# Kernel tuning notes

Hardware: AMD Instinct MI355X
Metric: run time of the kernel (lower is better)

Reference implementation:

```python
import jax, jax.numpy as jnp
import numpy as np

TEMPERATURE = 1.0
EPS = 1e-8
B, D, N, K = 2048, 32, 8192, 30


def setup_inputs() -> dict:
    key = jax.random.key(0)
    k1, k2, k3 = jax.random.split(key, 3)
    z_current = jax.random.normal(k1, (B, D), dtype=jnp.float32)
    pre_knn_indices = jax.random.randint(k2, (N, K), 0, N, dtype=jnp.int64 if jax.config.jax_enable_x64 else jnp.int32)
    sample_indices = jax.random.randint(k3, (B,), 0, N, dtype=jnp.int64 if jax.config.jax_enable_x64 else jnp.int32)
    return {"z_current": z_current, "pre_knn_indices": pre_knn_indices, "sample_indices": sample_indices}


def reference(z_current, pre_knn_indices, sample_indices):
    b = z_current.shape[0]
    eye = jnp.eye(b, dtype=bool)
    # pairwise Euclidean distance via gram trick: (B,B), avoids (B,B,D) intermediate
    sq = jnp.sum(z_current * z_current, axis=-1)
    d2 = jnp.maximum(sq[:, None] + sq[None, :] - 2.0 * (z_current @ z_current.T), 0.0)
    d2_safe = jnp.where(eye, 1.0, d2)  # avoid sqrt(0) on diagonal (masked below anyway)
    dist = jnp.sqrt(d2_safe)
    sim = jnp.where(eye, -jnp.inf, -dist / TEMPERATURE)
    soft_neighbors = jax.nn.softmax(sim, axis=1)  # (B,B)
    # neighbor mask: j is kept iff global id of j is in pre-kNN set of i, and j != i
    knn = pre_knn_indices[sample_indices]  # (B,K) global ids of i's pre-neighbors
    in_set = (knn[:, :, None] == sample_indices[None, None, :]).any(axis=1)  # (B,B)
    mask = in_set & ~eye
    s = jnp.sum(soft_neighbors * mask, axis=1)  # (B,)
    valid = mask.any(axis=1)
    count = valid.sum()
    loss_i = -jnp.log(s + EPS)
    total = jnp.sum(jnp.where(valid, loss_i, 0.0))
    return jnp.where(count > 0, total / count, jnp.float32(0.0))
```

## Files before the change

kernel.cpp:

```cpp
#include <hip/hip_runtime.h>
#include <math.h>

#define Bsz 2048
#define Ddim 32
#define Nsz 8192
#define Kk 30
#define TPB 256
#define ROWS 4
#define JSL 2
#define JTILE (Bsz / JSL)
#define JCH (JTILE / TPB)
#define NBLK ((Bsz / ROWS) * JSL)
#define NW (Nsz / 32)

__global__ __launch_bounds__(TPB, 2) void softnp_main(
    const float* __restrict__ z,
    const int*   __restrict__ pre_knn,
    const int*   __restrict__ samp,
    float*       __restrict__ wsden,
    float*       __restrict__ wsnum)
{
    __shared__ unsigned bits4[NW][ROWS];
    __shared__ int      sampsh[JTILE];
    __shared__ float    zish[ROWS * Ddim];
    __shared__ int      rowsi[ROWS];
    __shared__ float    rden[4][ROWS], rnum[4][ROWS];

    const int t  = threadIdx.x;
    const int rg = blockIdx.x >> 1;
    const int sl = blockIdx.x & 1;
    const int i0 = rg * ROWS;
    const int jb = sl * JTILE;

    #pragma unroll
    for (int c = 0; c < (NW * ROWS) / TPB; ++c)
        ((unsigned*)bits4)[t + c * TPB] = 0u;
    #pragma unroll
    for (int c = 0; c < JCH; ++c)
        sampsh[t + c * TPB] = samp[jb + t + c * TPB];
    if (t < ROWS * Ddim) zish[t] = z[(size_t)i0 * Ddim + t];
    if (t < ROWS) rowsi[t] = samp[i0 + t];
    __syncthreads();

    if (t < ROWS * 32) {
        const int r = t >> 5, k = t & 31;
        if (k < Kk) {
            const int id = pre_knn[(size_t)rowsi[r] * Kk + k];
            atomicOr(&bits4[id >> 5][r], 1u << (id & 31));
        }
    }

    float4 zi[ROWS][Ddim / 4];
    const float4* z4 = (const float4*)zish;
    #pragma unroll
    for (int r = 0; r < ROWS; ++r)
        #pragma unroll
        for (int d = 0; d < Ddim / 4; ++d)
            zi[r][d] = z4[r * (Ddim / 4) + d];

    float si2[ROWS];
    #pragma unroll
    for (int r = 0; r < ROWS; ++r) {
        float s = 0.f;
        #pragma unroll
        for (int d = 0; d < Ddim / 4; ++d)
            s += zi[r][d].x * zi[r][d].x + zi[r][d].y * zi[r][d].y
               + zi[r][d].z * zi[r][d].z + zi[r][d].w * zi[r][d].w;
        si2[r] = s;
    }
    __syncthreads();

    float den[ROWS] = {0.f, 0.f, 0.f, 0.f};
    float num[ROWS] = {0.f, 0.f, 0.f, 0.f};

    const float4* zg = (const float4*)z;
    int j = jb + t;
    float4 cur[8];
    #pragma unroll
    for (int d = 0; d < 8; ++d) cur[d] = zg[(size_t)j * 8 + d];

    #pragma unroll
    for (int c = 0; c < JCH; ++c) {
        float4 nxt[8];
        if (c + 1 < JCH) {
            #pragma unroll
            for (int d = 0; d < 8; ++d) nxt[d] = zg[(size_t)(j + TPB) * 8 + d];
        }

        float dot[ROWS] = {0.f, 0.f, 0.f, 0.f};
        float sj2 = 0.f;
        #pragma unroll
        for (int d = 0; d < 8; ++d) {
            const float4 v = cur[d];
            sj2 += v.x * v.x + v.y * v.y + v.z * v.z + v.w * v.w;
            #pragma unroll
            for (int r = 0; r < ROWS; ++r)
                dot[r] += zi[r][d].x * v.x + zi[r][d].y * v.y
                        + zi[r][d].z * v.z + zi[r][d].w * v.w;
        }

        const int   sj = sampsh[t + c * TPB];
        const uint4 bw = ((const uint4*)bits4)[sj >> 5];
        const unsigned bsel[4] = {bw.x, bw.y, bw.z, bw.w};
        #pragma unroll
        for (int r = 0; r < ROWS; ++r) {
            const float d2 = fmaxf(si2[r] + sj2 - 2.f * dot[r], 0.f);
            const bool diag = (j == i0 + r);
            const float e = diag ? 0.f : __expf(-sqrtf(d2));
            den[r] += e;
            if (!diag && ((bsel[r] >> (sj & 31)) & 1u)) num[r] += e;
        }

        if (c + 1 < JCH) {
            #pragma unroll
            for (int d = 0; d < 8; ++d) cur[d] = nxt[d];
        }
        j += TPB;
    }

    const int lane = t & 63, wv = t >> 6;
    #pragma unroll
    for (int r = 0; r < ROWS; ++r) {
        #pragma unroll
        for (int off = 32; off > 0; off >>= 1) {
            den[r] += __shfl_xor(den[r], off, 64);
            num[r] += __shfl_xor(num[r], off, 64);
        }
    }
    if (lane == 0) {
        #pragma unroll
        for (int r = 0; r < ROWS; ++r) { rden[wv][r] = den[r]; rnum[wv][r] = num[r]; }
    }
    __syncthreads();

    if (t < ROWS) {
        float D = 0.f, Nm = 0.f;
        #pragma unroll
        for (int w = 0; w < 4; ++w) { D += rden[w][t]; Nm += rnum[w][t]; }
        wsden[sl * Bsz + i0 + t] = D;
        wsnum[sl * Bsz + i0 + t] = Nm;
    }
}

__global__ __launch_bounds__(TPB) void softnp_final(
    const float* __restrict__ wsden,
    const float* __restrict__ wsnum,
    float*       __restrict__ out)
{
    __shared__ float rl[4], rc[4];
    const int t = threadIdx.x;
    float loss = 0.f, vcnt = 0.f;
    #pragma unroll
    for (int c = 0; c < Bsz / TPB; ++c) {
        const int r = t + c * TPB;
        const float D  = wsden[r] + wsden[Bsz + r];
        const float Nm = wsnum[r] + wsnum[Bsz + r];
        if (Nm > 0.f) {
            loss -= __logf(Nm / D + 1e-8f);
            vcnt += 1.f;
        }
    }
    #pragma unroll
    for (int off = 32; off > 0; off >>= 1) {
        loss += __shfl_xor(loss, off, 64);
        vcnt += __shfl_xor(vcnt, off, 64);
    }
    const int lane = t & 63, wv = t >> 6;
    if (lane == 0) { rl[wv] = loss; rc[wv] = vcnt; }
    __syncthreads();
    if (t == 0) {
        const float L = rl[0] + rl[1] + rl[2] + rl[3];
        const float C = rc[0] + rc[1] + rc[2] + rc[3];
        out[0] = (C > 0.f) ? L / C : 0.f;
    }
}

extern "C" void kernel_launch(void* const* d_in, const int* in_sizes, int n_in,
                              void* d_out, int out_size, void* d_ws, size_t ws_size,
                              hipStream_t stream)
{
    const float* z       = (const float*)d_in[0];
    const int*   pre_knn = (const int*)d_in[1];
    const int*   samp    = (const int*)d_in[2];
    float*       out     = (float*)d_out;
    float*       wsden   = (float*)d_ws;
    float*       wsnum   = wsden + JSL * Bsz;

    softnp_main<<<dim3(NBLK), dim3(TPB), 0, stream>>>(z, pre_knn, samp, wsden, wsnum);
    softnp_final<<<dim3(1), dim3(TPB), 0, stream>>>(wsden, wsnum, out);
}
```

Baseline: 85.55 us.

## Drop column split; compute per-row loss in main kernel, prefetch sample ids

Removes the two-way column split so each block covers all 2048 columns for its 4 rows. That halves the grid to 512 blocks and drops the redundant per-block bitmask build and z-row loads. The log-loss and valid count are now computed per row inside the main kernel and reduced per block, so the final kernel only sums 512 partials. Sample ids are prefetched from global memory into registers alongside z instead of being staged in shared memory. The trade-off is fewer blocks, which may underfill the 256 CUs on MI355X at 2 blocks per CU and lengthens each block's serial loop.

```diff
diff --git a/kernel.cpp b/kernel.cpp
--- a/kernel.cpp
+++ b/kernel.cpp
@@ -7,37 +7,28 @@
 #define Kk 30
 #define TPB 256
 #define ROWS 4
-#define JSL 2
-#define JTILE (Bsz / JSL)
-#define JCH (JTILE / TPB)
-#define NBLK ((Bsz / ROWS) * JSL)
+#define JCH (Bsz / TPB)
+#define NBLK (Bsz / ROWS)
 #define NW (Nsz / 32)
 
 __global__ __launch_bounds__(TPB, 2) void softnp_main(
     const float* __restrict__ z,
     const int*   __restrict__ pre_knn,
     const int*   __restrict__ samp,
-    float*       __restrict__ wsden,
-    float*       __restrict__ wsnum)
+    float*       __restrict__ wsloss,
+    float*       __restrict__ wscnt)
 {
     __shared__ unsigned bits4[NW][ROWS];
-    __shared__ int      sampsh[JTILE];
     __shared__ float    zish[ROWS * Ddim];
     __shared__ int      rowsi[ROWS];
     __shared__ float    rden[4][ROWS], rnum[4][ROWS];
 
     const int t  = threadIdx.x;
-    const int rg = blockIdx.x >> 1;
-    const int sl = blockIdx.x & 1;
-    const int i0 = rg * ROWS;
-    const int jb = sl * JTILE;
+    const int i0 = blockIdx.x * ROWS;
 
     #pragma unroll
     for (int c = 0; c < (NW * ROWS) / TPB; ++c)
         ((unsigned*)bits4)[t + c * TPB] = 0u;
-    #pragma unroll
-    for (int c = 0; c < JCH; ++c)
-        sampsh[t + c * TPB] = samp[jb + t + c * TPB];
     if (t < ROWS * Ddim) zish[t] = z[(size_t)i0 * Ddim + t];
     if (t < ROWS) rowsi[t] = samp[i0 + t];
     __syncthreads();
@@ -51,12 +42,12 @@
     }
 
     float4 zi[ROWS][Ddim / 4];
-    const float4* z4 = (const float4*)zish;
+    const float4* z4s = (const float4*)zish;
     #pragma unroll
     for (int r = 0; r < ROWS; ++r)
         #pragma unroll
         for (int d = 0; d < Ddim / 4; ++d)
-            zi[r][d] = z4[r * (Ddim / 4) + d];
+            zi[r][d] = z4s[r * (Ddim / 4) + d];
 
     float si2[ROWS];
     #pragma unroll
@@ -74,17 +65,20 @@
     float num[ROWS] = {0.f, 0.f, 0.f, 0.f};
 
     const float4* zg = (const float4*)z;
-    int j = jb + t;
+    int j = t;
     float4 cur[8];
     #pragma unroll
     for (int d = 0; d < 8; ++d) cur[d] = zg[(size_t)j * 8 + d];
+    int scur = samp[j];
 
     #pragma unroll
     for (int c = 0; c < JCH; ++c) {
         float4 nxt[8];
+        int snxt = 0;
         if (c + 1 < JCH) {
             #pragma unroll
             for (int d = 0; d < 8; ++d) nxt[d] = zg[(size_t)(j + TPB) * 8 + d];
+            snxt = samp[j + TPB];
         }
 
         float dot[ROWS] = {0.f, 0.f, 0.f, 0.f};
@@ -99,7 +93,7 @@
                         + zi[r][d].z * v.z + zi[r][d].w * v.w;
         }
 
-        const int   sj = sampsh[t + c * TPB];
+        const int   sj = scur;
         const uint4 bw = ((const uint4*)bits4)[sj >> 5];
         const unsigned bsel[4] = {bw.x, bw.y, bw.z, bw.w};
         #pragma unroll
@@ -114,6 +108,7 @@
         if (c + 1 < JCH) {
             #pragma unroll
             for (int d = 0; d < 8; ++d) cur[d] = nxt[d];
+            scur = snxt;
         }
         j += TPB;
     }
@@ -137,41 +132,38 @@
         float D = 0.f, Nm = 0.f;
         #pragma unroll
         for (int w = 0; w < 4; ++w) { D += rden[w][t]; Nm += rnum[w][t]; }
-        wsden[sl * Bsz + i0 + t] = D;
-        wsnum[sl * Bsz + i0 + t] = Nm;
+        float lr = 0.f, vr = 0.f;
+        if (Nm > 0.f) {
+            lr = -__logf(Nm / D + 1e-8f);
+            vr = 1.f;
+        }
+        lr += __shfl_xor(lr, 1, 64); vr += __shfl_xor(vr, 1, 64);
+        lr += __shfl_xor(lr, 2, 64); vr += __shfl_xor(vr, 2, 64);
+        if (t == 0) { wsloss[blockIdx.x] = lr; wscnt[blockIdx.x] = vr; }
     }
 }
 
 __global__ __launch_bounds__(TPB) void softnp_final(
-    const float* __restrict__ wsden,
-    const float* __restrict__ wsnum,
+    const float* __restrict__ wsloss,
+    const float* __restrict__ wscnt,
     float*       __restrict__ out)
 {
     __shared__ float rl[4], rc[4];
     const int t = threadIdx.x;
-    float loss = 0.f, vcnt = 0.f;
-    #pragma unroll
-    for (int c = 0; c < Bsz / TPB; ++c) {
-        const int r = t + c * TPB;
-        const float D  = wsden[r] + wsden[Bsz + r];
-        const float Nm = wsnum[r] + wsnum[Bsz + r];
-        if (Nm > 0.f) {
-            loss -= __logf(Nm / D + 1e-8f);
-            vcnt += 1.f;
-        }
-    }
+    float L = wsloss[t] + wsloss[t + TPB];
+    float C = wscnt[t] + wscnt[t + TPB];
     #pragma unroll
     for (int off = 32; off > 0; off >>= 1) {
-        loss += __shfl_xor(loss, off, 64);
-        vcnt += __shfl_xor(vcnt, off, 64);
+        L += __shfl_xor(L, off, 64);
+        C += __shfl_xor(C, off, 64);
     }
     const int lane = t & 63, wv = t >> 6;
-    if (lane == 0) { rl[wv] = loss; rc[wv] = vcnt; }
+    if (lane == 0) { rl[wv] = L; rc[wv] = C; }
     __syncthreads();
     if (t == 0) {
-        const float L = rl[0] + rl[1] + rl[2] + rl[3];
-        const float C = rc[0] + rc[1] + rc[2] + rc[3];
-        out[0] = (C > 0.f) ? L / C : 0.f;
+        const float Ls = rl[0] + rl[1] + rl[2] + rl[3];
+        const float Cs = rc[0] + rc[1] + rc[2] + rc[3];
+        out[0] = (Cs > 0.f) ? Ls / Cs : 0.f;
     }
 }
 
@@ -183,9 +175,9 @@
     const int*   pre_knn = (const int*)d_in[1];
     const int*   samp    = (const int*)d_in[2];
     float*       out     = (float*)d_out;
-    float*       wsden   = (float*)d_ws;
-    float*       wsnum   = wsden + JSL * Bsz;
+    float*       wsloss  = (float*)d_ws;
+    float*       wscnt   = wsloss + NBLK;
 
-    softnp_main<<<dim3(NBLK), dim3(TPB), 0, stream>>>(z, pre_knn, samp, wsden, wsnum);
-    softnp_final<<<dim3(1), dim3(TPB), 0, stream>>>(wsden, wsnum, out);
+    softnp_main<<<dim3(NBLK), dim3(TPB), 0, stream>>>(z, pre_knn, samp, wsloss, wscnt);
+    softnp_final<<<dim3(1), dim3(TPB), 0, stream>>>(wsloss, wscnt, out);
 }
```

New measurement: 77.02 us. 1.11x faster.

## Retile main kernel to 16 rows per block with single-column tiles and LDS transpose reduction

Applied to the files above, without the earlier changes.

Each block now handles 16 query rows against a 256-column slice split eight ways, so every thread processes exactly one column. The column loop and its prefetch disappear, and row vectors are read from shared memory instead of being held in registers. Per-row sums are built with a shared-memory transpose followed by a 16-lane shuffle, replacing the 64-lane shuffle per row. The goal is to amortize the bitmask build and column loads over more rows and to cut register pressure so occupancy can rise, at the cost of 16x more bitmask builds per row group and extra barriers and LDS traffic.

```diff
diff --git a/kernel.cpp b/kernel.cpp
--- a/kernel.cpp
+++ b/kernel.cpp
@@ -6,140 +6,125 @@
 #define Nsz 8192
 #define Kk 30
 #define TPB 256
-#define ROWS 4
-#define JSL 2
-#define JTILE (Bsz / JSL)
-#define JCH (JTILE / TPB)
+#define ROWS 16
+#define JSL 8
+#define JT (Bsz / JSL)
 #define NBLK ((Bsz / ROWS) * JSL)
 #define NW (Nsz / 32)
 
-__global__ __launch_bounds__(TPB, 2) void softnp_main(
+__global__ __launch_bounds__(TPB, 4) void softnp_main(
     const float* __restrict__ z,
     const int*   __restrict__ pre_knn,
     const int*   __restrict__ samp,
     float*       __restrict__ wsden,
     float*       __restrict__ wsnum)
 {
-    __shared__ unsigned bits4[NW][ROWS];
-    __shared__ int      sampsh[JTILE];
+    __shared__ unsigned bits[NW][ROWS];
     __shared__ float    zish[ROWS * Ddim];
+    __shared__ float    sish[ROWS];
     __shared__ int      rowsi[ROWS];
-    __shared__ float    rden[4][ROWS], rnum[4][ROWS];
 
     const int t  = threadIdx.x;
-    const int rg = blockIdx.x >> 1;
-    const int sl = blockIdx.x & 1;
-    const int i0 = rg * ROWS;
-    const int jb = sl * JTILE;
+    const int g  = blockIdx.x >> 3;
+    const int s  = blockIdx.x & 7;
+    const int i0 = g * ROWS;
+    const int j  = s * JT + t;
+
+    float4 zj[8];
+    const float4* zg = (const float4*)z;
+    #pragma unroll
+    for (int d = 0; d < 8; ++d) zj[d] = zg[(size_t)j * 8 + d];
+    const int sj = samp[j];
 
     #pragma unroll
     for (int c = 0; c < (NW * ROWS) / TPB; ++c)
-        ((unsigned*)bits4)[t + c * TPB] = 0u;
-    #pragma unroll
-    for (int c = 0; c < JCH; ++c)
-        sampsh[t + c * TPB] = samp[jb + t + c * TPB];
-    if (t < ROWS * Ddim) zish[t] = z[(size_t)i0 * Ddim + t];
+        ((unsigned*)bits)[t + c * TPB] = 0u;
+    zish[t]       = z[(size_t)i0 * Ddim + t];
+    zish[t + TPB] = z[(size_t)i0 * Ddim + t + TPB];
     if (t < ROWS) rowsi[t] = samp[i0 + t];
     __syncthreads();
 
-    if (t < ROWS * 32) {
-        const int r = t >> 5, k = t & 31;
-        if (k < Kk) {
+    #pragma unroll
+    for (int c = 0; c < 2; ++c) {
+        const int idx = t + c * TPB;
+        if (idx < ROWS * Kk) {
+            const int r  = idx / Kk, k = idx - r * Kk;
             const int id = pre_knn[(size_t)rowsi[r] * Kk + k];
-            atomicOr(&bits4[id >> 5][r], 1u << (id & 31));
+            atomicOr(&bits[id >> 5][r], 1u << (id & 31));
+        }
+    }
+    if (t < ROWS) {
+        float a = 0.f;
+        #pragma unroll
+        for (int d = 0; d < Ddim; ++d) {
+            const float w = zish[t * Ddim + d];
+            a += w * w;
+        }
+        sish[t] = a;
+    }
+    __syncthreads();
+
+    float dot[ROWS];
+    #pragma unroll
+    for (int r = 0; r < ROWS; ++r) dot[r] = 0.f;
+    float sj2 = 0.f;
+    const float4* z4s = (const float4*)zish;
+    #pragma unroll
+    for (int d = 0; d < 8; ++d) {
+        const float4 v = zj[d];
+        sj2 += v.x * v.x + v.y * v.y + v.z * v.z + v.w * v.w;
+        #pragma unroll
+        for (int r = 0; r < ROWS; ++r) {
+            const float4 w = z4s[r * 8 + d];
+            dot[r] += w.x * v.x + w.y * v.y + w.z * v.z + w.w * v.w;
         }
     }
 
-    float4 zi[ROWS][Ddim / 4];
-    const float4* z4 = (const float4*)zish;
+    const int wword = sj >> 5, wbit = sj & 31;
+    const uint4* b4 = (const uint4*)bits;
+    const uint4 q0 = b4[wword * 4 + 0], q1 = b4[wword * 4 + 1];
+    const uint4 q2 = b4[wword * 4 + 2], q3 = b4[wword * 4 + 3];
+    const unsigned bsel[ROWS] = {q0.x, q0.y, q0.z, q0.w, q1.x, q1.y, q1.z, q1.w,
+                                 q2.x, q2.y, q2.z, q2.w, q3.x, q3.y, q3.z, q3.w};
+    unsigned nmask = 0u;
+    const int dr = j - i0;
+    float dval[ROWS];
+    #pragma unroll
+    for (int r = 0; r < ROWS; ++r) {
+        const float d2 = fmaxf(sish[r] + sj2 - 2.f * dot[r], 0.f);
+        const bool diag = (r == dr);
+        const float e = diag ? 0.f : __expf(-sqrtf(d2));
+        dval[r] = e;
+        if (!diag && ((bsel[r] >> wbit) & 1u)) nmask |= 1u << r;
+    }
+
+    __syncthreads();
+    float* sc = (float*)bits;
+    const int gsel = t >> 4, m = t & 15;
+
+    #pragma unroll
+    for (int r = 0; r < ROWS; ++r) sc[r * TPB + t] = dval[r];
+    __syncthreads();
+    float a = 0.f;
+    #pragma unroll
+    for (int k = 0; k < 16; ++k)
+        a += sc[gsel * TPB + m * 16 + ((k + m) & 15)];
+    a += __shfl_xor(a, 1, 64); a += __shfl_xor(a, 2, 64);
+    a += __shfl_xor(a, 4, 64); a += __shfl_xor(a, 8, 64);
+    if (m == 0) wsden[s * Bsz + i0 + gsel] = a;
+
+    __syncthreads();
     #pragma unroll
     for (int r = 0; r < ROWS; ++r)
-        #pragma unroll
-        for (int d = 0; d < Ddim / 4; ++d)
-            zi[r][d] = z4[r * (Ddim / 4) + d];
-
-    float si2[ROWS];
+        sc[r * TPB + t] = ((nmask >> r) & 1u) ? dval[r] : 0.f;
+    __syncthreads();
+    float b = 0.f;
     #pragma unroll
-    for (int r = 0; r < ROWS; ++r) {
-        float s = 0.f;
-        #pragma unroll
-        for (int d = 0; d < Ddim / 4; ++d)
-            s += zi[r][d].x * zi[r][d].x + zi[r][d].y * zi[r][d].y
-               + zi[r][d].z * zi[r][d].z + zi[r][d].w * zi[r][d].w;
-        si2[r] = s;
-    }
-    __syncthreads();
-
-    float den[ROWS] = {0.f, 0.f, 0.f, 0.f};
-    float num[ROWS] = {0.f, 0.f, 0.f, 0.f};
-
-    const float4* zg = (const float4*)z;
-    int j = jb + t;
-    float4 cur[8];
-    #pragma unroll
-    for (int d = 0; d < 8; ++d) cur[d] = zg[(size_t)j * 8 + d];
-
-    #pragma unroll
-    for (int c = 0; c < JCH; ++c) {
-        float4 nxt[8];
-        if (c + 1 < JCH) {
-            #pragma unroll
-            for (int d = 0; d < 8; ++d) nxt[d] = zg[(size_t)(j + TPB) * 8 + d];
-        }
-
-        float dot[ROWS] = {0.f, 0.f, 0.f, 0.f};
-        float sj2 = 0.f;
-        #pragma unroll
-        for (int d = 0; d < 8; ++d) {
-            const float4 v = cur[d];
-            sj2 += v.x * v.x + v.y * v.y + v.z * v.z + v.w * v.w;
-            #pragma unroll
-            for (int r = 0; r < ROWS; ++r)
-                dot[r] += zi[r][d].x * v.x + zi[r][d].y * v.y
-                        + zi[r][d].z * v.z + zi[r][d].w * v.w;
-        }
-
-        const int   sj = sampsh[t + c * TPB];
-        const uint4 bw = ((const uint4*)bits4)[sj >> 5];
-        const unsigned bsel[4] = {bw.x, bw.y, bw.z, bw.w};
-        #pragma unroll
-        for (int r = 0; r < ROWS; ++r) {
-            const float d2 = fmaxf(si2[r] + sj2 - 2.f * dot[r], 0.f);
-            const bool diag = (j == i0 + r);
-            const float e = diag ? 0.f : __expf(-sqrtf(d2));
-            den[r] += e;
-            if (!diag && ((bsel[r] >> (sj & 31)) & 1u)) num[r] += e;
-        }
-
-        if (c + 1 < JCH) {
-            #pragma unroll
-            for (int d = 0; d < 8; ++d) cur[d] = nxt[d];
-        }
-        j += TPB;
-    }
-
-    const int lane = t & 63, wv = t >> 6;
-    #pragma unroll
-    for (int r = 0; r < ROWS; ++r) {
-        #pragma unroll
-        for (int off = 32; off > 0; off >>= 1) {
-            den[r] += __shfl_xor(den[r], off, 64);
-            num[r] += __shfl_xor(num[r], off, 64);
-        }
-    }
-    if (lane == 0) {
-        #pragma unroll
-        for (int r = 0; r < ROWS; ++r) { rden[wv][r] = den[r]; rnum[wv][r] = num[r]; }
-    }
-    __syncthreads();
-
-    if (t < ROWS) {
-        float D = 0.f, Nm = 0.f;
-        #pragma unroll
-        for (int w = 0; w < 4; ++w) { D += rden[w][t]; Nm += rnum[w][t]; }
-        wsden[sl * Bsz + i0 + t] = D;
-        wsnum[sl * Bsz + i0 + t] = Nm;
-    }
+    for (int k = 0; k < 16; ++k)
+        b += sc[gsel * TPB + m * 16 + ((k + m) & 15)];
+    b += __shfl_xor(b, 1, 64); b += __shfl_xor(b, 2, 64);
+    b += __shfl_xor(b, 4, 64); b += __shfl_xor(b, 8, 64);
+    if (m == 0) wsnum[s * Bsz + i0 + gsel] = b;
 }
 
 __global__ __launch_bounds__(TPB) void softnp_final(
@@ -152,11 +137,15 @@
     float loss = 0.f, vcnt = 0.f;
     #pragma unroll
     for (int c = 0; c < Bsz / TPB; ++c) {
-        const int r = t + c * TPB;
-        const float D  = wsden[r] + wsden[Bsz + r];
-        const float Nm = wsnum[r] + wsnum[Bsz + r];
-        if (Nm > 0.f) {
-            loss -= __logf(Nm / D + 1e-8f);
+        const int i = t + c * TPB;
+        float D = 0.f, N = 0.f;
+        #pragma unroll
+        for (int sl = 0; sl < JSL; ++sl) {
+            D += wsden[sl * Bsz + i];
+            N += wsnum[sl * Bsz + i];
+        }
+        if (N > 0.f) {
+            loss -= __logf(N / D + 1e-8f);
             vcnt += 1.f;
         }
     }
```

Measured after the change: 272.1 us. 218% more time.
